# Optimization experiments

Measured on AMD Instinct MI355X. Metric: run time of the kernel, lower is better.

The kernel has to match this reference:

```python
import math
import jax, jax.numpy as jnp
import numpy as np

HIDDEN = 1024
HEADS = 16
HEAD_DIM = HIDDEN // HEADS  # 64
SEQ = 4096
PATCH = 4064  # num rotated (patch) tokens; last PATCH positions get RoPE
EPS = 1e-6


def setup_inputs() -> dict:
    key = jax.random.key(0)
    ks = jax.random.split(key, 8)
    return {
        "x": jax.random.normal(ks[0], (1, SEQ, HIDDEN), dtype=jnp.float32),
        "rope_cos": jax.random.uniform(ks[1], (PATCH, HEAD_DIM // 2), dtype=jnp.float32),
        "rope_sin": jax.random.uniform(ks[2], (PATCH, HEAD_DIM // 2), dtype=jnp.float32),
        "wq": jax.random.normal(ks[3], (HIDDEN, HIDDEN), dtype=jnp.float32) / math.sqrt(HIDDEN),
        "wk": jax.random.normal(ks[4], (HIDDEN, HIDDEN), dtype=jnp.float32) / math.sqrt(HIDDEN),
        "wv": jax.random.normal(ks[5], (HIDDEN, HIDDEN), dtype=jnp.float32) / math.sqrt(HIDDEN),
        "wo": jax.random.normal(ks[6], (HIDDEN, HIDDEN), dtype=jnp.float32) / math.sqrt(HIDDEN),
        "q_norm_w": jnp.ones((HEAD_DIM,), dtype=jnp.float32),
        "k_norm_w": jnp.ones((HEAD_DIM,), dtype=jnp.float32),
    }


def _rms_norm(t, w):
    # RMSNorm over the last (head_dim) axis
    return t * jax.lax.rsqrt(jnp.mean(t * t, axis=-1, keepdims=True) + EPS) * w


def _apply_rope(t, cos, sin):
    # t: [b, s, h, d]; rotate only the last PATCH positions, pairwise complex mul
    b, s, h, d = t.shape
    P = cos.shape[0]
    tail = t[:, s - P:].reshape(b, P, h, d // 2, 2)
    x0, x1 = tail[..., 0], tail[..., 1]
    c = cos[None, :, None, :]
    sn = sin[None, :, None, :]
    rot = jnp.stack([x0 * c - x1 * sn, x0 * sn + x1 * c], axis=-1).reshape(b, P, h, d)
    return jnp.concatenate([t[:, : s - P], rot], axis=1)


def reference(x, rope_cos, rope_sin, wq, wk, wv, wo, q_norm_w, k_norm_w):
    b, s, _ = x.shape
    q = (x @ wq.T).reshape(b, s, HEADS, HEAD_DIM)
    k = (x @ wk.T).reshape(b, s, HEADS, HEAD_DIM)
    v = (x @ wv.T).reshape(b, s, HEADS, HEAD_DIM)
    q = _rms_norm(q, q_norm_w)
    k = _rms_norm(k, k_norm_w)
    q = _apply_rope(q, rope_cos, rope_sin)
    k = _apply_rope(k, rope_cos, rope_sin)
    q = q / math.sqrt(HEAD_DIM)
    scores = jnp.einsum('bqhd,bkhd->bhqk', q, k)
    attn = jax.nn.softmax(scores.astype(jnp.float32), axis=-1)
    out = jnp.einsum('bhqk,bkhd->bqhd', attn, v).reshape(b, s, HIDDEN)
    return out @ wo.T
```

## Files before the change

kernel.cpp:

```cpp
#include <hip/hip_runtime.h>
#include <hip/hip_bf16.h>
#include <stdint.h>

#define HIDDEN 1024
#define HEADS 16
#define HEAD_DIM 64
#define SEQ 4096
#define PATCH 4064
#define SKIP 32

typedef __attribute__((ext_vector_type(8))) short bf16x8;
typedef __attribute__((ext_vector_type(4))) float f32x4;
typedef __attribute__((ext_vector_type(2))) float f32x2;
typedef __attribute__((ext_vector_type(16))) float f32x16;

__device__ __forceinline__ float b2f(unsigned short u){
  union{uint32_t i; float f;} c; c.i = ((uint32_t)u)<<16; return c.f;
}
__device__ __forceinline__ unsigned short f2b(float f){
  union{float f; uint32_t i;} c; c.f=f;
  uint32_t r = c.i + 0x7fffu + ((c.i>>16)&1u);
  return (unsigned short)(r>>16);
}
__device__ __forceinline__ uint32_t cvtpk(float a, float b){
  uint32_t r;
  asm("v_cvt_pk_bf16_f32 %0, %1, %2" : "=v"(r) : "v"(a), "v"(b));
  return r;
}

#define GLD16(gp, lp) __builtin_amdgcn_global_load_lds( \
    (const __attribute__((address_space(1))) void*)(gp), \
    (__attribute__((address_space(3))) void*)(lp), 16, 0, 0)

__global__ __launch_bounds__(256) void convert_all(
    const float* __restrict__ x,  const float* __restrict__ wq,
    const float* __restrict__ wk, const float* __restrict__ wv,
    const float* __restrict__ wo,
    unsigned short* __restrict__ xb,  unsigned short* __restrict__ wqb,
    unsigned short* __restrict__ wkb, unsigned short* __restrict__ wvb,
    unsigned short* __restrict__ wob)
{
  size_t u = (size_t)blockIdx.x*256 + threadIdx.x;
  size_t e = u*8;
  const float* src; unsigned short* dst; size_t off;
  if      (e < 4194304ull) { src=x;  dst=xb;  off=e;            }
  else if (e < 5242880ull) { src=wq; dst=wqb; off=e-4194304ull; }
  else if (e < 6291456ull) { src=wk; dst=wkb; off=e-5242880ull; }
  else if (e < 7340032ull) { src=wv; dst=wvb; off=e-6291456ull; }
  else                     { src=wo; dst=wob; off=e-7340032ull; }
  float4 v0 = *(const float4*)(src+off);
  float4 v1 = *(const float4*)(src+off+4);
  union { bf16x8 v; unsigned short h[8]; } o;
  o.h[0]=f2b(v0.x); o.h[1]=f2b(v0.y); o.h[2]=f2b(v0.z); o.h[3]=f2b(v0.w);
  o.h[4]=f2b(v1.x); o.h[5]=f2b(v1.y); o.h[6]=f2b(v1.z); o.h[7]=f2b(v1.w);
  *(bf16x8*)(dst+off) = o.v;
}

__global__ __launch_bounds__(256) void gemm_qkv(
    const unsigned short* __restrict__ A,
    const unsigned short* __restrict__ B0,
    const unsigned short* __restrict__ B1,
    const unsigned short* __restrict__ B2,
    unsigned short* __restrict__ qout, unsigned short* __restrict__ kout,
    unsigned short* __restrict__ vout,
    const float* __restrict__ rc, const float* __restrict__ rs,
    const float* __restrict__ qw, const float* __restrict__ kw,
    int M, int Nper, int K)
{
  __shared__ unsigned short smem[16384];
  const int tid = threadIdx.x;
  const int w = tid>>6, l = tid&63;
  const int wm = w>>1, wn = w&1;
  const int g = l>>4, lr = l&15;
  const int bm = blockIdx.x;
  int bn = blockIdx.y;
  const int tilesPer = Nper >> 7;
  const int sel = bn / tilesPer;
  bn -= sel*tilesPer;
  const unsigned short* Bsel = (sel==0) ? B0 : ((sel==1) ? B1 : B2);

  const int off0 = w*1024 + l*16;
  const int r0 = off0>>6, c0 = (off0&63)>>1;
  const int off1 = off0 + 4096;
  const int r1 = off1>>6, c1 = (off1&63)>>1;

  const unsigned short* Ab = A    + (size_t)(bm*128)*K;
  const unsigned short* Bb = Bsel + (size_t)(bn*128)*K;

#define STG(db, kt) do { \
    GLD16(Ab + (size_t)r0*K + (kt) + c0, (char*)smem + (db) + off0); \
    GLD16(Ab + (size_t)r1*K + (kt) + c1, (char*)smem + (db) + off1); \
    GLD16(Bb + (size_t)r0*K + (kt) + c0, (char*)smem + (db) + 8192 + off0); \
    GLD16(Bb + (size_t)r1*K + (kt) + c1, (char*)smem + (db) + 8192 + off1); } while(0)

  f32x4 zero = {0.f,0.f,0.f,0.f};
  f32x4 acc[4][4];
  #pragma unroll
  for (int m=0;m<4;m++)
    #pragma unroll
    for (int n=0;n<4;n++) acc[m][n]=zero;

  const int nkt = K >> 5;
  STG(0, 0);
  for (int t = 0; t < nkt; ++t) {
    __syncthreads();
    const int db = (t&1)<<14;
    if (t+1 < nkt) STG(db^16384, (t+1)*32);
    bf16x8 a[4], b[4];
    #pragma unroll
    for (int m=0;m<4;m++)
      a[m] = *(const bf16x8*)((char*)smem + db + (wm*64 + m*16 + lr)*64 + g*16);
    #pragma unroll
    for (int n=0;n<4;n++)
      b[n] = *(const bf16x8*)((char*)smem + db + 8192 + (wn*64 + n*16 + lr)*64 + g*16);
    #pragma unroll
    for (int m=0;m<4;m++)
      #pragma unroll
      for (int n=0;n<4;n++)
        acc[m][n] = __builtin_amdgcn_mfma_f32_16x16x32_bf16(a[m], b[n], acc[m][n], 0,0,0);
  }
#undef STG

  if (sel <= 1) {
    const float* nw = (sel==0) ? qw : kw;
    unsigned short* dst = (sel==0) ? qout : kout;
    const float scl = (sel==0) ? 0.18033688011112042f : 1.0f;
    float wl[4];
    #pragma unroll
    for (int n=0;n<4;n++) wl[n] = nw[n*16+lr];
    const int hglob = bn*2 + wn;
    #pragma unroll
    for (int m=0;m<4;m++){
      const int rowb = bm*128 + wm*64 + m*16 + g*4;
      float rn[4];
      #pragma unroll
      for (int r=0;r<4;r++){
        float ss = 0.f;
        #pragma unroll
        for (int n=0;n<4;n++) ss += acc[m][n][r]*acc[m][n][r];
        ss += __shfl_xor(ss,1); ss += __shfl_xor(ss,2);
        ss += __shfl_xor(ss,4); ss += __shfl_xor(ss,8);
        rn[r] = rsqrtf(ss*(1.f/64.f) + 1e-6f);
      }
      #pragma unroll
      for (int r=0;r<4;r++){
        const int row = rowb + r;
        const int p = row - SKIP;
        #pragma unroll
        for (int n=0;n<4;n++){
          float v = acc[m][n][r]*rn[r]*wl[n];
          float c = 1.f, sn = 0.f;
          if (p >= 0){
            const int d2 = (n*16+lr)>>1;
            c  = rc[p*(HEAD_DIM/2) + d2];
            sn = rs[p*(HEAD_DIM/2) + d2];
          }
          const float partner = __shfl_xor(v, 1);
          const float o2 = (lr&1) ? (partner*sn + v*c) : (v*c - partner*sn);
          dst[(size_t)row*HIDDEN + hglob*64 + n*16 + lr] = f2b(o2*scl);
        }
      }
    }
  } else {
    #pragma unroll
    for (int m=0;m<4;m++){
      const int row = bm*128 + wm*64 + m*16 + g*4;
      #pragma unroll
      for (int n=0;n<4;n++){
        const int col = bn*128 + wn*64 + n*16 + lr;
        #pragma unroll
        for (int r=0;r<4;r++)
          vout[(size_t)(row+r)*HIDDEN + col] = f2b(acc[m][n][r]);
      }
    }
  }
}

__global__ __launch_bounds__(256) void gemm_out(
    const unsigned short* __restrict__ A,
    const unsigned short* __restrict__ B,
    float* __restrict__ Cf, int M, int N, int K)
{
  __shared__ unsigned short smem[12288];
  const int tid = threadIdx.x;
  const int w = tid>>6, l = tid&63;
  const int wm = w>>1, wn = w&1;
  const int g = l>>4, lr = l&15;
  const int bm = blockIdx.x;
  const int bn = blockIdx.y;

  const int off0 = w*1024 + l*16;
  const int r0 = off0>>6, c0 = (off0&63)>>1;
  const int off1 = off0 + 4096;
  const int r1 = off1>>6, c1 = (off1&63)>>1;
  const int offB = tid*16;
  const int rB = offB>>6, cB = (offB&63)>>1;

  const unsigned short* Ab = A + (size_t)(bm*128)*K;
  const unsigned short* Bb = B + (size_t)(bn*64)*K;

#define STG(db, kt) do { \
    GLD16(Ab + (size_t)r0*K + (kt) + c0, (char*)smem + (db) + off0); \
    GLD16(Ab + (size_t)r1*K + (kt) + c1, (char*)smem + (db) + off1); \
    GLD16(Bb + (size_t)rB*K + (kt) + cB, (char*)smem + (db) + 8192 + offB); } while(0)

  f32x4 zero = {0.f,0.f,0.f,0.f};
  f32x4 acc[4][2];
  #pragma unroll
  for (int m=0;m<4;m++)
    #pragma unroll
    for (int n=0;n<2;n++) acc[m][n]=zero;

  const int nkt = K >> 5;
  STG(0, 0);
  for (int t = 0; t < nkt; ++t) {
    __syncthreads();
    const int db = (t&1)*12288;
    if (t+1 < nkt) STG(db^12288, (t+1)*32);
    bf16x8 a[4], b[2];
    #pragma unroll
    for (int m=0;m<4;m++)
      a[m] = *(const bf16x8*)((char*)smem + db + (wm*64 + m*16 + lr)*64 + g*16);
    #pragma unroll
    for (int n=0;n<2;n++)
      b[n] = *(const bf16x8*)((char*)smem + db + 8192 + (wn*32 + n*16 + lr)*64 + g*16);
    #pragma unroll
    for (int m=0;m<4;m++)
      #pragma unroll
      for (int n=0;n<2;n++)
        acc[m][n] = __builtin_amdgcn_mfma_f32_16x16x32_bf16(a[m], b[n], acc[m][n], 0,0,0);
  }
#undef STG

  #pragma unroll
  for (int m=0;m<4;m++){
    const int row = bm*128 + wm*64 + m*16 + g*4;
    #pragma unroll
    for (int n=0;n<2;n++){
      const int col = bn*64 + wn*32 + n*16 + lr;
      #pragma unroll
      for (int r=0;r<4;r++)
        Cf[(size_t)(row+r)*N + col] = acc[m][n][r];
    }
  }
}

__global__ __launch_bounds__(256) void transpose_v(
    const unsigned short* __restrict__ v, unsigned short* __restrict__ vt)
{
  __shared__ unsigned short t[64*72];
  const int h = blockIdx.y;
  const int s0 = blockIdx.x * 64;
  const int tid = threadIdx.x;
  #pragma unroll
  for (int i=0;i<2;i++){
    const int e = tid + i*256;
    const int r = e>>3, cc = (e&7)*8;
    *(bf16x8*)&t[r*72+cc] = *(const bf16x8*)(v + (size_t)(s0+r)*HIDDEN + h*HEAD_DIM + cc);
  }
  __syncthreads();
  #pragma unroll
  for (int i=0;i<2;i++){
    const int e = tid + i*256;
    const int d = e>>3, sc = (e&7)*8;
    union { bf16x8 v8; unsigned short h8[8]; } o;
    #pragma unroll
    for (int j=0;j<8;j++){
      const int x  = sc + j;
      const int px = (x & ~12) | ((x&4)<<1) | ((x&8)>>1);
      o.h8[j] = t[px*72 + d];
    }
    *(bf16x8*)(vt + (size_t)(h*HEAD_DIM + d)*SEQ + s0 + sc) = o.v8;
  }
}

__device__ __forceinline__ void softmax_pack(f32x16 (&st)[2], f32x2 &lacc, bf16x8 (&pf)[4]){
  float pv[32];
  #pragma unroll
  for (int i=0;i<16;i++){
    pv[i]    = __builtin_amdgcn_exp2f(st[0][i]);
    pv[16+i] = __builtin_amdgcn_exp2f(st[1][i]);
  }
  #pragma unroll
  for (int i=0;i<8;i++){
    f32x2 a; a.x = pv[2*i];    a.y = pv[2*i+1];    lacc += a;
    f32x2 b; b.x = pv[16+2*i]; b.y = pv[16+2*i+1]; lacc += b;
  }
  #pragma unroll
  for (int t2=0; t2<2; t2++)
    #pragma unroll
    for (int e=0; e<2; e++){
      union { uint32_t u4[4]; bf16x8 v8; } pu;
      #pragma unroll
      for (int u=0; u<4; u++)
        pu.u4[u] = cvtpk(pv[t2*16+e*8+2*u], pv[t2*16+e*8+2*u+1]);
      pf[2*t2+e] = pu.v8;
    }
}

__global__ __launch_bounds__(512, 1) void attn_kernel(
    const unsigned short* __restrict__ q, const unsigned short* __restrict__ k,
    const unsigned short* __restrict__ vt, unsigned short* __restrict__ at)
{
  __shared__ unsigned short smem[32768];
  __shared__ float lsm[512];
  const int fid = blockIdx.x + 16*blockIdx.y;
  const int h  = (fid&7)*2 + ((fid>>3)&1);
  const int q0 = (fid>>4)*256;
  const int tid = threadIdx.x;
  const int half = tid>>8;
  const int ht = tid&255;
  const int w = (tid>>6)&3, l = tid&63;
  const int hi = l>>5, lo = l&31;
  const int NT = 32;
  const int tbase = half*NT;
  const int hbase = half*32768;

  const int cA = ht, cB = ht + 256;
  const int rA = cA>>3, rB = cB>>3;
  const int colA = ((cA&7)*16) ^ ((rA&7)<<4);
  const int colB = ((cB&7)*16) ^ ((rB&7)<<4);
  const unsigned short* kA = k  + (size_t)rA*HIDDEN + h*HEAD_DIM + (colA>>1);
  const unsigned short* kB = k  + (size_t)rB*HIDDEN + h*HEAD_DIM + (colB>>1);
  const unsigned short* vA = vt + ((size_t)(h*HEAD_DIM + rA))*SEQ + (colA>>1);
  const unsigned short* vB = vt + ((size_t)(h*HEAD_DIM + rB))*SEQ + (colB>>1);

#define STAGE(b, kOffE, vOffE) do { \
    GLD16(kA + (kOffE), (char*)smem + hbase + (b)*16384 + cA*16); \
    GLD16(kB + (kOffE), (char*)smem + hbase + (b)*16384 + cB*16); \
    GLD16(vA + (vOffE), (char*)smem + hbase + (b)*16384 + 8192 + cA*16); \
    GLD16(vB + (vOffE), (char*)smem + hbase + (b)*16384 + 8192 + cB*16); \
  } while(0)

  const int swz = (lo&7)<<4;
  int colo[4];
  #pragma unroll
  for (int ks=0; ks<4; ks++) colo[ks] = ((2*ks+hi)*16) ^ swz;

  bf16x8 qf0[4], qf1[4];
  {
    const unsigned short* qp = q + (size_t)(q0 + w*64 + lo)*HIDDEN + h*HEAD_DIM;
    #pragma unroll
    for (int ks=0; ks<4; ks++){
      qf0[ks] = *(const bf16x8*)(qp + ks*16 + hi*8);
      qf1[ks] = *(const bf16x8*)(qp + 32*HIDDEN + ks*16 + hi*8);
    }
  }

  f32x16 ot0[2], ot1[2];
  #pragma unroll
  for (int m2=0;m2<2;m2++)
    #pragma unroll
    for (int i=0;i<16;i++){ ot0[m2][i] = 0.f; ot1[m2][i] = 0.f; }
  f32x2 lacc0 = {0.f,0.f}, lacc1 = {0.f,0.f};

  STAGE(0, (size_t)tbase*64*HIDDEN, (size_t)tbase*64);

  for (int t = 0; t < NT; ++t) {
    __syncthreads();
    if (t+1 < NT) {
      const size_t ta = (size_t)(tbase + t + 1);
      STAGE((t+1)&1, ta*64*HIDDEN, ta*64);
    }
    const char* Kb = (const char*)smem + hbase + (t&1)*16384;
    const char* Vb = Kb + 8192;

    f32x16 st0[2], st1[2];
    __builtin_amdgcn_s_setprio(1);
    #pragma unroll
    for (int c=0;c<2;c++){
      #pragma unroll
      for (int i=0;i<16;i++){ st0[c][i] = 0.f; st1[c][i] = 0.f; }
      #pragma unroll
      for (int ks=0; ks<4; ks++){
        bf16x8 a = *(const bf16x8*)(Kb + (32*c+lo)*128 + colo[ks]);
        st0[c] = __builtin_amdgcn_mfma_f32_32x32x16_bf16(a, qf0[ks], st0[c], 0,0,0);
        st1[c] = __builtin_amdgcn_mfma_f32_32x32x16_bf16(a, qf1[ks], st1[c], 0,0,0);
      }
    }
    __builtin_amdgcn_s_setprio(0);

    bf16x8 pf0[4], pf1[4];
    softmax_pack(st0, lacc0, pf0);
    softmax_pack(st1, lacc1, pf1);

    __builtin_amdgcn_s_setprio(1);
    #pragma unroll
    for (int m2=0;m2<2;m2++)
      #pragma unroll
      for (int ks=0; ks<4; ks++){
        bf16x8 a = *(const bf16x8*)(Vb + (32*m2+lo)*128 + colo[ks]);
        ot0[m2] = __builtin_amdgcn_mfma_f32_32x32x16_bf16(a, pf0[ks], ot0[m2], 0,0,0);
        ot1[m2] = __builtin_amdgcn_mfma_f32_32x32x16_bf16(a, pf1[ks], ot1[m2], 0,0,0);
      }
    __builtin_amdgcn_s_setprio(0);
  }

  float ls0 = lacc0.x + lacc0.y;
  ls0 += __shfl_xor(ls0, 32);
  float ls1 = lacc1.x + lacc1.y;
  ls1 += __shfl_xor(ls1, 32);

  __syncthreads();
  if (hi == 0){
    lsm[half*256 + w*64 + lo]      = ls0;
    lsm[half*256 + w*64 + 32 + lo] = ls1;
  }
  #pragma unroll
  for (int m2=0;m2<2;m2++)
    #pragma unroll
    for (int f=0; f<4; f++)
      #pragma unroll
      for (int u=0; u<2; u++){
        const int d = 32*m2 + 8*f + 4*hi + 2*u;
        const uint32_t w0 = cvtpk(ot0[m2][4*f+2*u], ot0[m2][4*f+2*u+1]);
        *(uint32_t*)((char*)smem + hbase + (w*64+lo)*128 + ((d*2) ^ swz)) = w0;
        const uint32_t w1 = cvtpk(ot1[m2][4*f+2*u], ot1[m2][4*f+2*u+1]);
        *(uint32_t*)((char*)smem + hbase + (w*64+32+lo)*128 + ((d*2) ^ swz)) = w1;
      }
  __syncthreads();

  {
    const int ql = tid>>1, xh = tid&1;
    const float li = 1.0f / (lsm[ql] + lsm[256 + ql]);
    #pragma unroll
    for (int i=0;i<4;i++){
      const int cb = xh*64 + i*16;
      const int off = ql*128 + (cb ^ ((ql&7)<<4));
      union { bf16x8 v; unsigned short s[8]; } a, b, o;
      a.v = *(const bf16x8*)((const char*)smem + off);
      b.v = *(const bf16x8*)((const char*)smem + 32768 + off);
      #pragma unroll
      for (int j=0;j<8;j++)
        o.s[j] = f2b((b2f(a.s[j]) + b2f(b.s[j])) * li);
      *(bf16x8*)(at + (size_t)(q0+ql)*HIDDEN + h*HEAD_DIM + (cb>>1)) = o.v;
    }
  }
#undef STAGE
}

extern "C" void kernel_launch(void* const* d_in, const int* in_sizes, int n_in,
                              void* d_out, int out_size, void* d_ws, size_t ws_size,
                              hipStream_t stream)
{
  const float* x  = (const float*)d_in[0];
  const float* rc = (const float*)d_in[1];
  const float* rs = (const float*)d_in[2];
  const float* wq = (const float*)d_in[3];
  const float* wk = (const float*)d_in[4];
  const float* wv = (const float*)d_in[5];
  const float* wo = (const float*)d_in[6];
  const float* qw = (const float*)d_in[7];
  const float* kw = (const float*)d_in[8];
  float* out = (float*)d_out;

  char* ws = (char*)d_ws;
  const size_t MB = 1024*1024;
  unsigned short* xb  = (unsigned short*)(ws + 0);
  unsigned short* wqb = (unsigned short*)(ws + 8*MB);
  unsigned short* wkb = (unsigned short*)(ws + 10*MB);
  unsigned short* wvb = (unsigned short*)(ws + 12*MB);
  unsigned short* wob = (unsigned short*)(ws + 14*MB);
  unsigned short* qkv = (unsigned short*)(ws + 16*MB);
  unsigned short* qb = qkv;
  unsigned short* kb = qkv + (size_t)SEQ*HIDDEN;
  unsigned short* vb = qkv + (size_t)2*SEQ*HIDDEN;
  unsigned short* vt = (unsigned short*)(ws + 0);
  unsigned short* at = (unsigned short*)(ws + 40*MB);

  convert_all<<<4096, 256, 0, stream>>>(x, wq, wk, wv, wo, xb, wqb, wkb, wvb, wob);
  gemm_qkv<<<dim3(32,24), 256, 0, stream>>>(
      xb, wqb, wkb, wvb, qb, kb, vb, rc, rs, qw, kw, SEQ, HIDDEN, HIDDEN);
  transpose_v<<<dim3(64,16), 256, 0, stream>>>(vb, vt);
  attn_kernel<<<dim3(16,16), 512, 0, stream>>>(qb, kb, vt, at);
  gemm_out<<<dim3(32,16), 256, 0, stream>>>(at, wob, out, SEQ, HIDDEN, HIDDEN);
}
```

Measured before the change: 150.1 us.

## Fuse V transpose into QKV GEMM epilogue via shared-memory staging

The V-projection epilogue of the QKV GEMM now stages each warp's 64x64 tile in shared memory and writes it out already transposed, with the permuted column order that attention expects. The separate transpose_v kernel is removed. This saves a launch and a full round trip of V through global memory. In exchange the GEMM needs a slightly larger shared buffer and extra syncs in the epilogue.

```diff
diff --git a/kernel.cpp b/kernel.cpp
--- a/kernel.cpp
+++ b/kernel.cpp
@@ -62,12 +62,12 @@
     const unsigned short* __restrict__ B1,
     const unsigned short* __restrict__ B2,
     unsigned short* __restrict__ qout, unsigned short* __restrict__ kout,
-    unsigned short* __restrict__ vout,
+    unsigned short* __restrict__ vtout,
     const float* __restrict__ rc, const float* __restrict__ rs,
     const float* __restrict__ qw, const float* __restrict__ kw,
     int M, int Nper, int K)
 {
-  __shared__ unsigned short smem[16384];
+  __shared__ unsigned short smem[16896];
   const int tid = threadIdx.x;
   const int w = tid>>6, l = tid&63;
   const int wm = w>>1, wn = w&1;
@@ -162,16 +162,30 @@
       }
     }
   } else {
-    #pragma unroll
-    for (int m=0;m<4;m++){
-      const int row = bm*128 + wm*64 + m*16 + g*4;
-      #pragma unroll
-      for (int n=0;n<4;n++){
-        const int col = bn*128 + wn*64 + n*16 + lr;
+    const int hglob = bn*2 + wn;
+    const int sbase = bm*128 + wm*64;
+    unsigned short* lchunk = smem + w*4224;
+    __syncthreads();
+    #pragma unroll
+    for (int m=0;m<4;m++)
+      #pragma unroll
+      for (int n=0;n<4;n++)
         #pragma unroll
         for (int r=0;r<4;r++)
-          vout[(size_t)(row+r)*HIDDEN + col] = f2b(acc[m][n][r]);
-      }
+          lchunk[(m*16 + g*4 + r)*66 + n*16 + lr] = f2b(acc[m][n][r]);
+    __syncthreads();
+    #pragma unroll
+    for (int i=0;i<8;i++){
+      const int e = i*64 + l;
+      const int d = e>>3, sc = (e&7)*8;
+      union { bf16x8 v8; unsigned short h8[8]; } o;
+      #pragma unroll
+      for (int j=0;j<8;j++){
+        const int x  = sc + j;
+        const int px = (x & ~12) | ((x&4)<<1) | ((x&8)>>1);
+        o.h8[j] = lchunk[px*66 + d];
+      }
+      *(bf16x8*)(vtout + (size_t)(hglob*HEAD_DIM + d)*SEQ + sbase + sc) = o.v8;
     }
   }
 }
@@ -242,35 +256,6 @@
       for (int r=0;r<4;r++)
         Cf[(size_t)(row+r)*N + col] = acc[m][n][r];
     }
-  }
-}
-
-__global__ __launch_bounds__(256) void transpose_v(
-    const unsigned short* __restrict__ v, unsigned short* __restrict__ vt)
-{
-  __shared__ unsigned short t[64*72];
-  const int h = blockIdx.y;
-  const int s0 = blockIdx.x * 64;
-  const int tid = threadIdx.x;
-  #pragma unroll
-  for (int i=0;i<2;i++){
-    const int e = tid + i*256;
-    const int r = e>>3, cc = (e&7)*8;
-    *(bf16x8*)&t[r*72+cc] = *(const bf16x8*)(v + (size_t)(s0+r)*HIDDEN + h*HEAD_DIM + cc);
-  }
-  __syncthreads();
-  #pragma unroll
-  for (int i=0;i<2;i++){
-    const int e = tid + i*256;
-    const int d = e>>3, sc = (e&7)*8;
-    union { bf16x8 v8; unsigned short h8[8]; } o;
-    #pragma unroll
-    for (int j=0;j<8;j++){
-      const int x  = sc + j;
-      const int px = (x & ~12) | ((x&4)<<1) | ((x&8)>>1);
-      o.h8[j] = t[px*72 + d];
-    }
-    *(bf16x8*)(vt + (size_t)(h*HEAD_DIM + d)*SEQ + s0 + sc) = o.v8;
   }
 }
 
@@ -464,14 +449,12 @@
   unsigned short* qkv = (unsigned short*)(ws + 16*MB);
   unsigned short* qb = qkv;
   unsigned short* kb = qkv + (size_t)SEQ*HIDDEN;
-  unsigned short* vb = qkv + (size_t)2*SEQ*HIDDEN;
-  unsigned short* vt = (unsigned short*)(ws + 0);
+  unsigned short* vt = (unsigned short*)(ws + 32*MB);
   unsigned short* at = (unsigned short*)(ws + 40*MB);
 
   convert_all<<<4096, 256, 0, stream>>>(x, wq, wk, wv, wo, xb, wqb, wkb, wvb, wob);
   gemm_qkv<<<dim3(32,24), 256, 0, stream>>>(
-      xb, wqb, wkb, wvb, qb, kb, vb, rc, rs, qw, kw, SEQ, HIDDEN, HIDDEN);
-  transpose_v<<<dim3(64,16), 256, 0, stream>>>(vb, vt);
+      xb, wqb, wkb, wvb, qb, kb, vt, rc, rs, qw, kw, SEQ, HIDDEN, HIDDEN);
   attn_kernel<<<dim3(16,16), 512, 0, stream>>>(qb, kb, vt, at);
   gemm_out<<<dim3(32,16), 256, 0, stream>>>(at, wob, out, SEQ, HIDDEN, HIDDEN);
 }
```

New measurement: 151.3 us. No clear change (+0.8%).
